# Performance work log

Hardware: AMD Instinct MI355X
Metric: run time of the kernel (lower is better)

The kernel has to match this reference:

```python
import jax, jax.numpy as jnp
import numpy as np

M = 4096   # nodes per layer (also number of input nodes)
L = 32     # internal layers
K = 64     # in-degree of each internal node


def setup_inputs() -> dict:
    key = jax.random.key(0)
    k_x, k_wi, k_bi, k_w, k_b, k_g = jax.random.split(key, 6)
    x = jax.random.normal(k_x, (M, 1), dtype=jnp.float32)
    w_in = jax.random.normal(k_wi, (M, 1), dtype=jnp.float32)
    b_in = jax.random.normal(k_bi, (M,), dtype=jnp.float32)
    # scale internal weights so sigmoid(K-term dot) is not fully saturated
    w = jax.random.normal(k_w, (L, M, K), dtype=jnp.float32) * 0.05
    b = jax.random.normal(k_b, (L, M), dtype=jnp.float32)
    # predecessor indices into the previous layer's value vector
    igraf = jax.random.randint(k_g, (L, M, K), 0, M, dtype=jnp.int32)
    return {"x": x, "w_in": w_in, "b_in": b_in, "w": w, "b": b, "igraf": igraf}


def reference(x, w_in, b_in, w, b, igraf):
    # input nodes: relu(Linear(1,1)) applied to each scalar input, vectorized
    v = jax.nn.relu(w_in[:, 0] * x[:, 0] + b_in)          # [M]
    # internal nodes, layer by layer (topological order):
    # each node gathers K predecessor values and applies sigmoid(Linear(K,1))
    for l in range(L):
        g = v[igraf[l]]                                   # [M, K] irregular gather
        v = jax.nn.sigmoid(jnp.einsum('mk,mk->m', w[l], g) + b[l])
    # original returns values[n_nodes - 1] (shape [1])
    return v[-1:]
```

## Files before the change

kernel.cpp:

```cpp
#include <hip/hip_runtime.h>

#define M 4096
#define L 32
#define K 64
#define NBLK 256
#define BLOCK 256
#define NPW 4
#define NPB 16
#define MK (M * K)
#define FB 0xAAAAAAAAu

__global__ __launch_bounds__(BLOCK)
void net_kernel(const float* __restrict__ x,
                const float* __restrict__ w_in,
                const float* __restrict__ b_in,
                const float* __restrict__ w,
                const float* __restrict__ b,
                const int* __restrict__ igraf,
                float* __restrict__ out,
                unsigned long long* __restrict__ buf)
{
    __shared__ float sv[M];

    const int tid  = threadIdx.x;
    const int blk  = blockIdx.x;
    const int wave = tid >> 6;
    const int lane = tid & 63;
    const int base = blk * NPB + wave * NPW;
    const bool lastblk = (blk == NBLK - 1);

    float wv[NPW]; int iv[NPW]; float breg = 0.0f;
    {
        const size_t b0 = (size_t)base * K + (size_t)lane;
        #pragma unroll
        for (int j = 0; j < NPW; ++j) {
            wv[j] = w[b0 + (size_t)j * K];
            iv[j] = igraf[b0 + (size_t)j * K];
        }
        if (lane < NPW) breg = b[base + lane];
    }

    #pragma unroll
    for (int j = 0; j < 4; ++j) {
        const int idx = tid + j * BLOCK;
        const float4 x4 = ((const float4*)x)[idx];
        const float4 wi = ((const float4*)w_in)[idx];
        const float4 bi = ((const float4*)b_in)[idx];
        float4 r;
        r.x = fmaxf(fmaf(wi.x, x4.x, bi.x), 0.0f);
        r.y = fmaxf(fmaf(wi.y, x4.y, bi.y), 0.0f);
        r.z = fmaxf(fmaf(wi.z, x4.z, bi.z), 0.0f);
        r.w = fmaxf(fmaf(wi.w, x4.w, bi.w), 0.0f);
        ((float4*)sv)[idx] = r;
    }
    __syncthreads();

    for (int l = 0; l < L; ++l) {
        float p[NPW];
        #pragma unroll
        for (int j = 0; j < NPW; ++j) p[j] = wv[j] * sv[iv[j]];

        #pragma unroll
        for (int j = 0; j < NPW; ++j) {
            #pragma unroll
            for (int off = 32; off > 0; off >>= 1)
                p[j] += __shfl_xor(p[j], off, 64);
        }

        float pj = p[0];
        pj = (lane == 1) ? p[1] : pj;
        pj = (lane == 2) ? p[2] : pj;
        pj = (lane == 3) ? p[3] : pj;
        const float val = 1.0f / (1.0f + __expf(-(pj + breg)));

        if (l == L - 1) {
            if (wave == 3 && lane == 3) out[0] = val;
            break;
        }

        const unsigned tag = FB + (unsigned)(l + 1);
        unsigned long long* bufr = buf + (size_t)((l + 1) & 1) * M;

        if (lane < NPW) {
            const unsigned long long pk =
                ((unsigned long long)tag << 32) |
                (unsigned long long)__float_as_uint(val);
            __hip_atomic_store(&bufr[base + lane], pk,
                               __ATOMIC_RELAXED, __HIP_MEMORY_SCOPE_AGENT);
        }

        if ((l == L - 2) && !lastblk) return;

        if ((l + 2 < L) || lastblk) {
            const size_t nb = (size_t)(l + 1) * MK + (size_t)base * K + (size_t)lane;
            #pragma unroll
            for (int j = 0; j < NPW; ++j) {
                wv[j] = w[nb + (size_t)j * K];
                iv[j] = igraf[nb + (size_t)j * K];
            }
            if (lane < NPW) breg = b[(l + 1) * M + base + lane];
        }

        unsigned long long vals[16];
        #pragma unroll
        for (int j = 0; j < 16; ++j)
            vals[j] = __hip_atomic_load(&bufr[tid + j * BLOCK],
                                        __ATOMIC_RELAXED,
                                        __HIP_MEMORY_SCOPE_AGENT);

        __syncthreads();

        for (;;) {
            bool ok = true;
            #pragma unroll
            for (int j = 0; j < 16; ++j) {
                if ((unsigned)(vals[j] >> 32) != tag) {
                    ok = false;
                    vals[j] = __hip_atomic_load(&bufr[tid + j * BLOCK],
                                                __ATOMIC_RELAXED,
                                                __HIP_MEMORY_SCOPE_AGENT);
                }
            }
            if (ok) break;
            __builtin_amdgcn_s_sleep(1);
        }

        #pragma unroll
        for (int j = 0; j < 16; ++j)
            sv[tid + j * BLOCK] = __uint_as_float((unsigned)vals[j]);
        __syncthreads();
    }
}

extern "C" void kernel_launch(void* const* d_in, const int* in_sizes, int n_in,
                              void* d_out, int out_size, void* d_ws, size_t ws_size,
                              hipStream_t stream) {
    const float* x     = (const float*)d_in[0];
    const float* w_in  = (const float*)d_in[1];
    const float* b_in  = (const float*)d_in[2];
    const float* wt    = (const float*)d_in[3];
    const float* b     = (const float*)d_in[4];
    const int*   igraf = (const int*)d_in[5];
    float*       out   = (float*)d_out;

    unsigned long long* buf = (unsigned long long*)d_ws;

    hipLaunchKernelGGL(net_kernel, dim3(NBLK), dim3(BLOCK), 0, stream,
                       x, w_in, b_in, wt, b, igraf, out, buf);
    (void)in_sizes; (void)n_in; (void)out_size; (void)ws_size;
}
```

Before: 178.0 us.

## Replace block-wide layer broadcast with per-wave dataflow gathers from global buffer

Each wave now gathers only its K predecessor values straight from the tagged global buffer and spins on those entries alone. This replaces copying the whole 4096-entry layer into shared memory with block barriers. The ring buffer grows from 2 to 8 layer slots so that waves running at different layers do not overwrite values still being read. The input layer is computed on the fly from gathered x/w_in/b_in, and next-layer weights are prefetched into registers. This removes __syncthreads and full-vector loads per layer but adds scattered atomic global loads and depends on waves never running more than a few layers apart.

```diff
diff --git a/kernel.cpp b/kernel.cpp
--- a/kernel.cpp
+++ b/kernel.cpp
@@ -6,7 +6,6 @@
 #define NBLK 256
 #define BLOCK 256
 #define NPW 4
-#define NPB 16
 #define MK (M * K)
 #define FB 0xAAAAAAAAu
 
@@ -20,14 +19,12 @@
                 float* __restrict__ out,
                 unsigned long long* __restrict__ buf)
 {
-    __shared__ float sv[M];
-
     const int tid  = threadIdx.x;
     const int blk  = blockIdx.x;
     const int wave = tid >> 6;
     const int lane = tid & 63;
-    const int base = blk * NPB + wave * NPW;
-    const bool lastblk = (blk == NBLK - 1);
+    const int base = blk * 16 + wave * NPW;
+    const bool finwave = (blk == NBLK - 1) && (wave == 3);
 
     float wv[NPW]; int iv[NPW]; float breg = 0.0f;
     {
@@ -40,95 +37,122 @@
         if (lane < NPW) breg = b[base + lane];
     }
 
+    float gx[NPW], gw[NPW], gb[NPW];
     #pragma unroll
-    for (int j = 0; j < 4; ++j) {
-        const int idx = tid + j * BLOCK;
-        const float4 x4 = ((const float4*)x)[idx];
-        const float4 wi = ((const float4*)w_in)[idx];
-        const float4 bi = ((const float4*)b_in)[idx];
-        float4 r;
-        r.x = fmaxf(fmaf(wi.x, x4.x, bi.x), 0.0f);
-        r.y = fmaxf(fmaf(wi.y, x4.y, bi.y), 0.0f);
-        r.z = fmaxf(fmaf(wi.z, x4.z, bi.z), 0.0f);
-        r.w = fmaxf(fmaf(wi.w, x4.w, bi.w), 0.0f);
-        ((float4*)sv)[idx] = r;
+    for (int j = 0; j < NPW; ++j) {
+        const int idx = iv[j];
+        gw[j] = w_in[idx];
+        gx[j] = x[idx];
+        gb[j] = b_in[idx];
     }
-    __syncthreads();
 
-    for (int l = 0; l < L; ++l) {
+    float wn[NPW]; int in2[NPW]; float bn = 0.0f;
+    {
+        const size_t nb = (size_t)1 * MK + (size_t)base * K + (size_t)lane;
+        #pragma unroll
+        for (int j = 0; j < NPW; ++j) {
+            wn[j]  = w[nb + (size_t)j * K];
+            in2[j] = igraf[nb + (size_t)j * K];
+        }
+        if (lane < NPW) bn = b[1 * M + base + lane];
+    }
+
+    {
         float p[NPW];
         #pragma unroll
-        for (int j = 0; j < NPW; ++j) p[j] = wv[j] * sv[iv[j]];
-
+        for (int j = 0; j < NPW; ++j)
+            p[j] = wv[j] * fmaxf(fmaf(gw[j], gx[j], gb[j]), 0.0f);
         #pragma unroll
         for (int j = 0; j < NPW; ++j) {
             #pragma unroll
             for (int off = 32; off > 0; off >>= 1)
                 p[j] += __shfl_xor(p[j], off, 64);
         }
+        float pj = p[0];
+        pj = (lane == 1) ? p[1] : pj;
+        pj = (lane == 2) ? p[2] : pj;
+        pj = (lane == 3) ? p[3] : pj;
+        const float val = 1.0f / (1.0f + __expf(-(pj + breg)));
+        if (lane < NPW) {
+            const unsigned long long pk =
+                ((unsigned long long)(FB + 1u) << 32) |
+                (unsigned long long)__float_as_uint(val);
+            __hip_atomic_store(&buf[(size_t)1 * M + base + lane], pk,
+                               __ATOMIC_RELAXED, __HIP_MEMORY_SCOPE_AGENT);
+        }
+        #pragma unroll
+        for (int j = 0; j < NPW; ++j) { wv[j] = wn[j]; iv[j] = in2[j]; }
+        breg = bn;
+    }
 
+    for (int s = 2; s <= L; ++s) {
+        const unsigned tag = FB + (unsigned)(s - 1);
+        unsigned long long* src = buf + (size_t)((s - 1) & 7) * M;
+
+        unsigned long long g[NPW];
+        #pragma unroll
+        for (int j = 0; j < NPW; ++j)
+            g[j] = __hip_atomic_load(&src[iv[j]], __ATOMIC_RELAXED,
+                                     __HIP_MEMORY_SCOPE_AGENT);
+
+        if (s < L) {
+            const size_t nb = (size_t)s * MK + (size_t)base * K + (size_t)lane;
+            #pragma unroll
+            for (int j = 0; j < NPW; ++j) {
+                wn[j]  = w[nb + (size_t)j * K];
+                in2[j] = igraf[nb + (size_t)j * K];
+            }
+            if (lane < NPW) bn = b[s * M + base + lane];
+        }
+
+        for (;;) {
+            bool ok = true;
+            #pragma unroll
+            for (int j = 0; j < NPW; ++j) {
+                if ((unsigned)(g[j] >> 32) != tag) {
+                    ok = false;
+                    g[j] = __hip_atomic_load(&src[iv[j]], __ATOMIC_RELAXED,
+                                             __HIP_MEMORY_SCOPE_AGENT);
+                }
+            }
+            if (ok) break;
+            __builtin_amdgcn_s_sleep(1);
+        }
+
+        float p[NPW];
+        #pragma unroll
+        for (int j = 0; j < NPW; ++j)
+            p[j] = wv[j] * __uint_as_float((unsigned)g[j]);
+        #pragma unroll
+        for (int j = 0; j < NPW; ++j) {
+            #pragma unroll
+            for (int off = 32; off > 0; off >>= 1)
+                p[j] += __shfl_xor(p[j], off, 64);
+        }
         float pj = p[0];
         pj = (lane == 1) ? p[1] : pj;
         pj = (lane == 2) ? p[2] : pj;
         pj = (lane == 3) ? p[3] : pj;
         const float val = 1.0f / (1.0f + __expf(-(pj + breg)));
 
-        if (l == L - 1) {
-            if (wave == 3 && lane == 3) out[0] = val;
+        if (s == L) {
+            if (lane == 3) out[0] = val;
             break;
         }
 
-        const unsigned tag = FB + (unsigned)(l + 1);
-        unsigned long long* bufr = buf + (size_t)((l + 1) & 1) * M;
-
         if (lane < NPW) {
             const unsigned long long pk =
-                ((unsigned long long)tag << 32) |
+                ((unsigned long long)(FB + (unsigned)s) << 32) |
                 (unsigned long long)__float_as_uint(val);
-            __hip_atomic_store(&bufr[base + lane], pk,
+            __hip_atomic_store(&buf[(size_t)(s & 7) * M + base + lane], pk,
                                __ATOMIC_RELAXED, __HIP_MEMORY_SCOPE_AGENT);
         }
 
-        if ((l == L - 2) && !lastblk) return;
-
-        if ((l + 2 < L) || lastblk) {
-            const size_t nb = (size_t)(l + 1) * MK + (size_t)base * K + (size_t)lane;
-            #pragma unroll
-            for (int j = 0; j < NPW; ++j) {
-                wv[j] = w[nb + (size_t)j * K];
-                iv[j] = igraf[nb + (size_t)j * K];
-            }
-            if (lane < NPW) breg = b[(l + 1) * M + base + lane];
-        }
-
-        unsigned long long vals[16];
-        #pragma unroll
-        for (int j = 0; j < 16; ++j)
-            vals[j] = __hip_atomic_load(&bufr[tid + j * BLOCK],
-                                        __ATOMIC_RELAXED,
-                                        __HIP_MEMORY_SCOPE_AGENT);
-
-        __syncthreads();
-
-        for (;;) {
-            bool ok = true;
-            #pragma unroll
-            for (int j = 0; j < 16; ++j) {
-                if ((unsigned)(vals[j] >> 32) != tag) {
-                    ok = false;
-                    vals[j] = __hip_atomic_load(&bufr[tid + j * BLOCK],
-                                                __ATOMIC_RELAXED,
-                                                __HIP_MEMORY_SCOPE_AGENT);
-                }
-            }
-            if (ok) break;
-            __builtin_amdgcn_s_sleep(1);
-        }
+        if (s == L - 1 && !finwave) return;
 
         #pragma unroll
-        for (int j = 0; j < 16; ++j)
-            sv[tid + j * BLOCK] = __uint_as_float((unsigned)vals[j]);
-        __syncthreads();
+        for (int j = 0; j < NPW; ++j) { wv[j] = wn[j]; iv[j] = in2[j]; }
+        breg = bn;
     }
 }
 
```

Measured after the change: 203.4 us. 1.14x slower.

## Add per-block flag barrier with replicated flags and multi-slot value ring

Applied to the files above, without the earlier changes.

Before the data spin, each block now publishes a layer counter to eight replicated flag arrays, and one wave polls its replica for all 256 blocks. Only after that does it read the 4096 tagged values with plain loads, keeping the tag check as a fallback. Value buffers become a ring of up to 32 slots chosen by workspace size, so fast blocks cannot overwrite values that slow blocks still need. The aim is to cut polling traffic on the 32 KB value buffer, at the cost of an extra block barrier and flag stores per layer.

```diff
diff --git a/kernel.cpp b/kernel.cpp
--- a/kernel.cpp
+++ b/kernel.cpp
@@ -10,6 +10,8 @@
 #define MK (M * K)
 #define FB 0xAAAAAAAAu
 
+typedef unsigned long long u64;
+
 __global__ __launch_bounds__(BLOCK)
 void net_kernel(const float* __restrict__ x,
                 const float* __restrict__ w_in,
@@ -18,7 +20,9 @@
                 const float* __restrict__ b,
                 const int* __restrict__ igraf,
                 float* __restrict__ out,
-                unsigned long long* __restrict__ buf)
+                unsigned* __restrict__ flags,
+                u64* __restrict__ bufs,
+                unsigned ringmask)
 {
     __shared__ float sv[M];
 
@@ -46,12 +50,12 @@
         const float4 x4 = ((const float4*)x)[idx];
         const float4 wi = ((const float4*)w_in)[idx];
         const float4 bi = ((const float4*)b_in)[idx];
-        float4 r;
-        r.x = fmaxf(fmaf(wi.x, x4.x, bi.x), 0.0f);
-        r.y = fmaxf(fmaf(wi.y, x4.y, bi.y), 0.0f);
-        r.z = fmaxf(fmaf(wi.z, x4.z, bi.z), 0.0f);
-        r.w = fmaxf(fmaf(wi.w, x4.w, bi.w), 0.0f);
-        ((float4*)sv)[idx] = r;
+        float4 rr;
+        rr.x = fmaxf(fmaf(wi.x, x4.x, bi.x), 0.0f);
+        rr.y = fmaxf(fmaf(wi.y, x4.y, bi.y), 0.0f);
+        rr.z = fmaxf(fmaf(wi.z, x4.z, bi.z), 0.0f);
+        rr.w = fmaxf(fmaf(wi.w, x4.w, bi.w), 0.0f);
+        ((float4*)sv)[idx] = rr;
     }
     __syncthreads();
 
@@ -75,24 +79,56 @@
 
         if (l == L - 1) {
             if (wave == 3 && lane == 3) out[0] = val;
-            break;
+            return;
         }
 
-        const unsigned tag = FB + (unsigned)(l + 1);
-        unsigned long long* bufr = buf + (size_t)((l + 1) & 1) * M;
+        const unsigned r = (unsigned)(l + 1);
+        u64* bufr = bufs + (size_t)(r & ringmask) * M;
 
         if (lane < NPW) {
-            const unsigned long long pk =
-                ((unsigned long long)tag << 32) |
-                (unsigned long long)__float_as_uint(val);
+            const u64 pk = ((u64)(FB + r) << 32) |
+                           (u64)__float_as_uint(val);
             __hip_atomic_store(&bufr[base + lane], pk,
                                __ATOMIC_RELAXED, __HIP_MEMORY_SCOPE_AGENT);
         }
+        __syncthreads();
 
-        if ((l == L - 2) && !lastblk) return;
+        if (tid == 0) {
+            #pragma unroll
+            for (int rep = 0; rep < 8; ++rep)
+                __hip_atomic_store(&flags[rep * 256 + blk], r,
+                                   __ATOMIC_RELAXED,
+                                   __HIP_MEMORY_SCOPE_AGENT);
+        }
+
+        if (l == L - 2 && !lastblk) return;
+
+        if (wave == 0) {
+            const unsigned* rp = flags + (blk & 7) * 256;
+            for (;;) {
+                bool ok = true;
+                #pragma unroll
+                for (int j = 0; j < 4; ++j) {
+                    const unsigned f = __hip_atomic_load(
+                        &rp[lane + j * 64], __ATOMIC_RELAXED,
+                        __HIP_MEMORY_SCOPE_AGENT);
+                    ok &= (f >= r) & (f <= (unsigned)L);
+                }
+                if (__ballot(ok) == ~0ull) break;
+                __builtin_amdgcn_s_sleep(2);
+            }
+        }
+        __syncthreads();
+
+        u64 vals[16];
+        #pragma unroll
+        for (int j = 0; j < 16; ++j)
+            vals[j] = bufr[tid + j * BLOCK];
+        __asm__ volatile("" ::: "memory");
 
         if ((l + 2 < L) || lastblk) {
-            const size_t nb = (size_t)(l + 1) * MK + (size_t)base * K + (size_t)lane;
+            const size_t nb = (size_t)(l + 1) * MK
+                            + (size_t)base * K + (size_t)lane;
             #pragma unroll
             for (int j = 0; j < NPW; ++j) {
                 wv[j] = w[nb + (size_t)j * K];
@@ -101,15 +137,7 @@
             if (lane < NPW) breg = b[(l + 1) * M + base + lane];
         }
 
-        unsigned long long vals[16];
-        #pragma unroll
-        for (int j = 0; j < 16; ++j)
-            vals[j] = __hip_atomic_load(&bufr[tid + j * BLOCK],
-                                        __ATOMIC_RELAXED,
-                                        __HIP_MEMORY_SCOPE_AGENT);
-
-        __syncthreads();
-
+        const unsigned tag = FB + r;
         for (;;) {
             bool ok = true;
             #pragma unroll
@@ -143,9 +171,16 @@
     const int*   igraf = (const int*)d_in[5];
     float*       out   = (float*)d_out;
 
-    unsigned long long* buf = (unsigned long long*)d_ws;
+    unsigned* flags = (unsigned*)d_ws;
+    u64*      bufs  = (u64*)((char*)d_ws + 16384);
+
+    const size_t bufbytes = (size_t)M * sizeof(u64);
+    unsigned ringmask;
+    if      (ws_size >= 16384 + 32 * bufbytes) ringmask = 31u;
+    else if (ws_size >= 16384 +  8 * bufbytes) ringmask = 7u;
+    else                                       ringmask = 1u;
 
     hipLaunchKernelGGL(net_kernel, dim3(NBLK), dim3(BLOCK), 0, stream,
-                       x, w_in, b_in, wt, b, igraf, out, buf);
+                       x, w_in, b_in, wt, b, igraf, out, flags, bufs, ringmask);
     (void)in_sizes; (void)n_in; (void)out_size; (void)ws_size;
 }
```

Result: slower. 206.9 us (+16.2%).
